# Kernel optimization log

Measured on AMD Instinct MI355X. Metric: run time of the kernel, lower is better.

## Reference

```python
import jax, jax.numpy as jnp
import numpy as np

M = 1536   # rows (users)
N = 1536   # cols (items)
P_ROW = 4  # Chebyshev order over rows
P_COL = 4  # Chebyshev order over cols
OUT = 32   # out_channels_GCCN


def cheb_basis(L, order):
    """Stack of Chebyshev polynomials T_k(L), shape (order+1, n, n)."""
    n = L.shape[0]
    Ts = [jnp.eye(n, dtype=L.dtype)]
    if order > 0:
        Ts.append(L)
    for _ in range(2, order + 1):
        Ts.append(2.0 * (L @ Ts[-1]) - Ts[-2])
    return jnp.stack(Ts)


def setup_inputs() -> dict:
    key = jax.random.key(0)
    kx, kr, kc, kt = jax.random.split(key, 4)
    x = jax.random.normal(kx, (1, M, N), dtype=jnp.float32)
    # Scaled symmetric 'Laplacians' with spectral radius < 1 so the
    # Chebyshev recursion stays numerically stable.
    Ar = jax.random.normal(kr, (M, M), dtype=jnp.float32)
    Lr = (Ar + Ar.T) / (4.0 * jnp.sqrt(jnp.float32(M)))
    Ac = jax.random.normal(kc, (N, N), dtype=jnp.float32)
    Lc = (Ac + Ac.T) / (4.0 * jnp.sqrt(jnp.float32(N)))
    theta = jax.random.normal(kt, (P_ROW + 1, P_COL + 1, 1, OUT), dtype=jnp.float32) * 0.05
    bias = jnp.zeros((OUT,), dtype=jnp.float32)
    return {"x": x, "Lr": Lr, "Lc": Lc, "theta": theta, "bias": bias}


def reference(x, Lr, Lc, theta, bias):
    # Chebyshev bases: Tr (p_row+1, M, M), Tc (p_col+1, N, N)
    Tr = cheb_basis(Lr, theta.shape[0] - 1)
    Tc = cheb_basis(Lc, theta.shape[1] - 1)
    # Stage 1: row transform -> (i, c, M, N)
    x_row = jnp.einsum('imp,cpn->icmn', Tr, x)
    # Stage 2: col transform -> (i, j, c, M, N)
    basis_feats = jnp.einsum('icmn,jnk->ijcmk', x_row, Tc)
    # Stage 3: bilinear weights -> (OUT, M, N)
    out = jnp.einsum('ijcmn,ijco->omn', basis_feats, theta)
    return out + bias[:, None, None]
```

## Files before the change

### kernel.cpp

```cpp
#include <hip/hip_runtime.h>
#include <hip/hip_bf16.h>


#define NDIM 1536
#define PM (NDIM * NDIM)
#define NK 24

typedef __attribute__((ext_vector_type(8))) short bf16x8;
typedef __attribute__((ext_vector_type(4))) float f32x4;

__device__ inline void gload_lds16(const void* g, void* l) {
  __builtin_amdgcn_global_load_lds(
      (const __attribute__((address_space(1))) void*)g,
      (__attribute__((address_space(3))) void*)l, 16, 0, 0);
}

__device__ inline unsigned short f2bf(float f) {
  __hip_bfloat16 h = __float2bfloat16(f);
  return *reinterpret_cast<unsigned short*>(&h);
}
__device__ inline float bf2f(unsigned short u) {
  return __uint_as_float((unsigned)u << 16);
}

struct ZSet {
  const unsigned short* A;
  const unsigned short* Bt;
  unsigned short* out;
  const unsigned short* Cp;
  int mode;
};
struct ZSet4 { ZSet z[4]; };

#define PH_MID()                                       \
  do {                                                 \
    asm volatile("" ::: "memory");                     \
    __builtin_amdgcn_s_barrier();                      \
    asm volatile("s_waitcnt lgkmcnt(0)" ::: "memory"); \
    __builtin_amdgcn_sched_barrier(0);                 \
    __builtin_amdgcn_s_setprio(1);                     \
  } while (0)

#define PH_END()                                       \
  do {                                                 \
    __builtin_amdgcn_s_setprio(0);                     \
    asm volatile("" ::: "memory");                     \
    __builtin_amdgcn_s_barrier();                      \
  } while (0)

__global__ __launch_bounds__(512, 2) void gemm256_k(ZSet4 zs) {
  const ZSet zp = zs.z[blockIdx.z];
  __shared__ __align__(16) unsigned short As[2][2][8192];
  __shared__ __align__(16) unsigned short Bs[2][2][8192];
  const int tid = threadIdx.x;
  const int lane = tid & 63;
  const int wave = tid >> 6;
  const int wm = wave >> 2, wn = wave & 3;
  const int gm0 = blockIdx.y * 256;
  const int jn = blockIdx.x / 6;
  const int nloc0 = (blockIdx.x % 6) * 256;
  const int q = lane >> 4;
  const int rowl = lane & 15;
  const unsigned short* Ab = zp.A;
  const unsigned short* Btb = zp.Bt + (size_t)jn * PM;
  unsigned short* outb = zp.out + (size_t)jn * 5 * PM;

  bf16x8 a[4][2];
  bf16x8 b0[2][2], b1[2][2];
  f32x4 acc00[4][2] = {}, acc01[4][2] = {}, acc10[4][2] = {}, acc11[4][2] = {};

  auto stageA = [&](int buf, int h, int kt) {
#pragma unroll
    for (int l = 0; l < 2; ++l) {
      const int o = (wave * 2 + l) * 1024 + lane * 16;
      const int wms = o >> 13;
      const int r = (o >> 7) & 63;
      const int s = (o >> 4) & 7;
      const unsigned short* src =
          Ab + (size_t)(gm0 + wms * 128 + h * 64 + r) * NDIM + kt * 64 +
          ((s ^ (r & 7)) << 3);
      gload_lds16(src, &As[buf][h][(wave * 2 + l) * 512]);
    }
  };
  auto stageB = [&](int buf, int h, int kt) {
#pragma unroll
    for (int l = 0; l < 2; ++l) {
      const int o = (wave * 2 + l) * 1024 + lane * 16;
      const int wns = o >> 12;
      const int r = (o >> 7) & 31;
      const int s = (o >> 4) & 7;
      const unsigned short* src =
          Btb + (size_t)(nloc0 + wns * 64 + h * 32 + r) * NDIM + kt * 64 +
          ((s ^ (r & 7)) << 3);
      gload_lds16(src, &Bs[buf][h][(wave * 2 + l) * 512]);
    }
  };
  auto loadA = [&](int buf, int h) {
#pragma unroll
    for (int mt = 0; mt < 4; ++mt) {
      const int lr = mt * 16 + rowl;
#pragma unroll
      for (int ks = 0; ks < 2; ++ks) {
        const int s0 = ks * 4 + q;
        a[mt][ks] = *(const bf16x8*)&As[buf][h][wm * 4096 + lr * 64 +
                                                ((s0 ^ (lr & 7)) << 3)];
      }
    }
  };
  auto loadB = [&](bf16x8 (&bb)[2][2], int buf, int h) {
#pragma unroll
    for (int nt = 0; nt < 2; ++nt) {
      const int lr = nt * 16 + rowl;
#pragma unroll
      for (int ks = 0; ks < 2; ++ks) {
        const int s0 = ks * 4 + q;
        bb[nt][ks] = *(const bf16x8*)&Bs[buf][h][wn * 2048 + lr * 64 +
                                                 ((s0 ^ (lr & 7)) << 3)];
      }
    }
  };
  auto mfma16 = [&](f32x4 (&ac)[4][2], bf16x8 (&bb)[2][2]) {
#pragma unroll
    for (int mt = 0; mt < 4; ++mt)
#pragma unroll
      for (int nt = 0; nt < 2; ++nt)
#pragma unroll
        for (int ks = 0; ks < 2; ++ks)
          ac[mt][nt] = __builtin_amdgcn_mfma_f32_16x16x32_bf16(
              a[mt][ks], bb[nt][ks], ac[mt][nt], 0, 0, 0);
  };

  stageA(0, 0, 0); stageB(0, 0, 0); stageB(0, 1, 0); stageA(0, 1, 0);
  stageA(1, 0, 1); stageB(1, 0, 1); stageB(1, 1, 1);
  asm volatile("s_waitcnt vmcnt(6)" ::: "memory");
  __builtin_amdgcn_s_barrier();

  auto ktile = [&](int kt, int b) {
    loadA(b, 0);
    loadB(b0, b, 0);
    if (kt + 1 < NK) stageA(b ^ 1, 1, kt + 1);
    PH_MID();
    mfma16(acc00, b0);
    PH_END();
    loadB(b1, b, 1);
    if (kt + 2 < NK) stageA(b, 0, kt + 2);
    PH_MID();
    mfma16(acc01, b1);
    PH_END();
    loadA(b, 1);
    if (kt + 2 < NK) stageB(b, 0, kt + 2);
    PH_MID();
    mfma16(acc11, b1);
    PH_END();
    if (kt + 2 < NK) {
      stageB(b, 1, kt + 2);
      asm volatile("s_waitcnt vmcnt(6)" ::: "memory");
    } else {
      asm volatile("s_waitcnt vmcnt(0)" ::: "memory");
    }
    PH_MID();
    mfma16(acc10, b0);
    PH_END();
  };
  for (int kt = 0; kt < NK; kt += 2) {
    ktile(kt, 0);
    ktile(kt + 1, 1);
  }

  auto writeQ = [&](f32x4 (&ac)[4][2], int mh, int nh) {
#pragma unroll
    for (int mt = 0; mt < 4; ++mt)
#pragma unroll
      for (int nt = 0; nt < 2; ++nt)
#pragma unroll
        for (int v = 0; v < 4; ++v) {
          const int row = gm0 + wm * 128 + mh * 64 + mt * 16 + q * 4 + v;
          const int col = nloc0 + wn * 64 + nh * 32 + nt * 16 + rowl;
          const size_t idx = (size_t)row * NDIM + col;
          float val = ac[mt][nt][v];
          if (zp.mode == 1) val = 2.0f * val - bf2f(zp.Cp[idx]);
          if (zp.mode == 2) val = 2.0f * val - (row == col ? 1.0f : 0.0f);
          outb[idx] = f2bf(val);
        }
  };
  writeQ(acc00, 0, 0);
  writeQ(acc01, 0, 1);
  writeQ(acc11, 1, 1);
  writeQ(acc10, 1, 0);
}

__global__ __launch_bounds__(256) void gemm_k(ZSet4 zs) {
  const ZSet zp = zs.z[blockIdx.z];
  __shared__ __align__(16) unsigned short As[128 * 32];
  __shared__ __align__(16) unsigned short Bs[128 * 32];
  const int tid = threadIdx.x;
  const int lane = tid & 63;
  const int wave = tid >> 6;
  const int wm = wave >> 1, wn = wave & 1;
  const int gm0 = blockIdx.y * 128;
  const int jn = blockIdx.x / 12;
  const int nloc0 = (blockIdx.x % 12) * 128;
  const int q = lane >> 4;
  const int rowl = lane & 15;

  const unsigned short* Btb = zp.Bt + (size_t)jn * PM;
  unsigned short* outb = zp.out + (size_t)jn * 5 * PM;

  f32x4 acc[4][4] = {};

  for (int k0 = 0; k0 < NDIM; k0 += 32) {
#pragma unroll
    for (int l = 0; l < 2; ++l) {
      int f = l * 256 + wave * 64 + lane;
      int r = f >> 2, kc = f & 3;
      const unsigned short* ga = zp.A + (size_t)(gm0 + r) * NDIM + k0 + kc * 8;
      const unsigned short* gb = Btb + (size_t)(nloc0 + r) * NDIM + k0 + kc * 8;
      unsigned short* la = &As[(size_t)(l * 256 + wave * 64) * 8];
      unsigned short* lb = &Bs[(size_t)(l * 256 + wave * 64) * 8];
      gload_lds16(ga, la);
      gload_lds16(gb, lb);
    }
    __syncthreads();
    bf16x8 af[4], bfv[4];
#pragma unroll
    for (int t = 0; t < 4; ++t) {
      af[t] = *(const bf16x8*)&As[(wm * 64 + t * 16 + rowl) * 32 + q * 8];
      bfv[t] = *(const bf16x8*)&Bs[(wn * 64 + t * 16 + rowl) * 32 + q * 8];
    }
#pragma unroll
    for (int mt = 0; mt < 4; ++mt)
#pragma unroll
      for (int nt = 0; nt < 4; ++nt)
        acc[mt][nt] = __builtin_amdgcn_mfma_f32_16x16x32_bf16(
            af[mt], bfv[nt], acc[mt][nt], 0, 0, 0);
    __syncthreads();
  }

#pragma unroll
  for (int mt = 0; mt < 4; ++mt) {
#pragma unroll
    for (int nt = 0; nt < 4; ++nt) {
#pragma unroll
      for (int v = 0; v < 4; ++v) {
        int row = gm0 + wm * 64 + mt * 16 + q * 4 + v;
        int col = nloc0 + wn * 64 + nt * 16 + rowl;
        size_t idx = (size_t)row * NDIM + col;
        float val = acc[mt][nt][v];
        if (zp.mode == 1) val = 2.0f * val - bf2f(zp.Cp[idx]);
        if (zp.mode == 2) val = 2.0f * val - (row == col ? 1.0f : 0.0f);
        outb[idx] = f2bf(val);
      }
    }
  }
}

__global__ void transpose_f2b(const float* __restrict__ in,
                              unsigned short* __restrict__ out16,
                              unsigned short* __restrict__ outS) {
  __shared__ float tile[32][33];
  int bx = blockIdx.x, by = blockIdx.y;
  int tx = threadIdx.x;
#pragma unroll
  for (int r = threadIdx.y; r < 32; r += 8) {
    float v = in[(size_t)(by * 32 + r) * NDIM + bx * 32 + tx];
    tile[r][tx] = v;
    outS[(size_t)(by * 32 + r) * NDIM + bx * 32 + tx] = f2bf(v);
  }
  __syncthreads();
  int ox = by * 32 + tx;
#pragma unroll
  for (int r = threadIdx.y; r < 32; r += 8)
    out16[(size_t)(bx * 32 + r) * NDIM + ox] = f2bf(tile[tx][r]);
}

__global__ void cast_bf16_k(const float* __restrict__ in,
                            unsigned short* __restrict__ out) {
  int i = (blockIdx.x * 256 + threadIdx.x) * 4;
  float4 v = *(const float4*)(in + i);
  ushort4 r;
  r.x = f2bf(v.x); r.y = f2bf(v.y); r.z = f2bf(v.z); r.w = f2bf(v.w);
  *(ushort4*)(out + i) = r;
}

__global__ __launch_bounds__(256, 2) void combine_k(
    const unsigned short* __restrict__ Z,
    const float* __restrict__ theta,
    const float* __restrict__ bias,
    float* __restrict__ out) {
  __shared__ float th[800];
  __shared__ float bs[32];
  const int tid = threadIdx.x;
  for (int t = tid; t < 800; t += 256) th[t] = theta[t];
  if (tid < 32) bs[tid] = bias[tid];
  __syncthreads();

  const size_t p0 = (size_t)(blockIdx.x * 256 + tid) * 4;
  float z[25][4];
#pragma unroll
  for (int c = 0; c < 25; ++c) {
    uint2 u = *(const uint2*)(Z + (size_t)c * PM + p0);
    z[c][0] = __uint_as_float(u.x << 16);
    z[c][1] = __uint_as_float(u.x & 0xffff0000u);
    z[c][2] = __uint_as_float(u.y << 16);
    z[c][3] = __uint_as_float(u.y & 0xffff0000u);
  }
#pragma unroll 2
  for (int o = 0; o < 32; ++o) {
    float b = bs[o];
    float a0 = b, a1 = b, a2 = b, a3 = b;
#pragma unroll
    for (int c = 0; c < 25; ++c) {
      const int i = c % 5, j = c / 5;
      float t = th[i * 160 + j * 32 + o];
      a0 += t * z[c][0];
      a1 += t * z[c][1];
      a2 += t * z[c][2];
      a3 += t * z[c][3];
    }
    float4 w; w.x = a0; w.y = a1; w.z = a2; w.w = a3;
    *(float4*)(out + (size_t)o * PM + p0) = w;
  }
}

extern "C" void kernel_launch(void* const* d_in, const int* in_sizes, int n_in,
                              void* d_out, int out_size, void* d_ws, size_t ws_size,
                              hipStream_t stream) {
  (void)in_sizes; (void)n_in; (void)out_size; (void)ws_size;
  const float* X = (const float*)d_in[0];
  const float* Lr = (const float*)d_in[1];
  const float* Lc = (const float*)d_in[2];
  const float* theta = (const float*)d_in[3];
  const float* bias = (const float*)d_in[4];
  float* out = (float*)d_out;

  unsigned short* Zall = (unsigned short*)d_ws;
  unsigned short* Tr = Zall + (size_t)25 * PM;
  unsigned short* Tc = Tr + (size_t)4 * PM;
  unsigned short* Xt = Tc + (size_t)4 * PM;

  unsigned short* Tr0 = Tr;                 unsigned short* Tc0 = Tc;
  unsigned short* Tr1 = Tr + (size_t)PM;    unsigned short* Tc1 = Tc + (size_t)PM;
  unsigned short* Tr2 = Tr + (size_t)2*PM;  unsigned short* Tc2 = Tc + (size_t)2*PM;
  unsigned short* Tr3 = Tr + (size_t)3*PM;  unsigned short* Tc3 = Tc + (size_t)3*PM;

  cast_bf16_k<<<PM / 1024, 256, 0, stream>>>(Lr, Tr0);
  cast_bf16_k<<<PM / 1024, 256, 0, stream>>>(Lc, Tc0);
  transpose_f2b<<<dim3(48, 48), dim3(32, 8), 0, stream>>>(X, Xt, Zall);

  {
    ZSet4 a{};
    a.z[0] = {Tr0, Tr0, Tr1, nullptr, 2};
    a.z[1] = {Tc0, Tc0, Tc1, nullptr, 2};
    gemm_k<<<dim3(12, 12, 2), 256, 0, stream>>>(a);
  }
  {
    ZSet4 a{};
    a.z[0] = {Tr0, Tr1, Tr2, Tr0, 1};
    a.z[1] = {Tr1, Tr1, Tr3, nullptr, 2};
    a.z[2] = {Tc0, Tc1, Tc2, Tc0, 1};
    a.z[3] = {Tc1, Tc1, Tc3, nullptr, 2};
    gemm_k<<<dim3(12, 12, 4), 256, 0, stream>>>(a);
  }
  {
    ZSet4 a{};
    a.z[0] = {Tr, Xt, Zall + (size_t)PM, nullptr, 0};
    gemm256_k<<<dim3(6, 24, 1), 512, 0, stream>>>(a);
  }
  {
    ZSet4 a{};
    a.z[0] = {Zall, Tc0, Zall + (size_t)5 * PM, nullptr, 0};
    gemm256_k<<<dim3(24, 30, 1), 512, 0, stream>>>(a);
  }

  combine_k<<<PM / 1024, 256, 0, stream>>>(Zall, theta, bias, out);
}
```

Baseline: 716.5 us.

## Swizzle GEMM blocks across XCDs, merge cast launches, slim combine registers

Result: slower. 993.9 us (+38.7%).

```diff
diff --git a/kernel.cpp b/kernel.cpp
--- a/kernel.cpp
+++ b/kernel.cpp
@@ -32,6 +32,16 @@
 };
 struct ZSet4 { ZSet z[4]; };
 
+__device__ inline void xcd_swizzle(int& bx, int& by) {
+  const int gx = gridDim.x;
+  const int nwg = gx * gridDim.y;
+  int lin = by * gx + bx;
+  const int nper = nwg >> 3;
+  lin = (lin & 7) * nper + (lin >> 3);
+  bx = lin % gx;
+  by = lin / gx;
+}
+
 #define PH_MID()                                       \
   do {                                                 \
     asm volatile("" ::: "memory");                     \
@@ -52,13 +62,15 @@
   const ZSet zp = zs.z[blockIdx.z];
   __shared__ __align__(16) unsigned short As[2][2][8192];
   __shared__ __align__(16) unsigned short Bs[2][2][8192];
+  int bswx = blockIdx.x, bswy = blockIdx.y;
+  xcd_swizzle(bswx, bswy);
   const int tid = threadIdx.x;
   const int lane = tid & 63;
   const int wave = tid >> 6;
   const int wm = wave >> 2, wn = wave & 3;
-  const int gm0 = blockIdx.y * 256;
-  const int jn = blockIdx.x / 6;
-  const int nloc0 = (blockIdx.x % 6) * 256;
+  const int gm0 = bswy * 256;
+  const int jn = bswx / 6;
+  const int nloc0 = (bswx % 6) * 256;
   const int q = lane >> 4;
   const int rowl = lane & 15;
   const unsigned short* Ab = zp.A;
@@ -193,13 +205,15 @@
   const ZSet zp = zs.z[blockIdx.z];
   __shared__ __align__(16) unsigned short As[128 * 32];
   __shared__ __align__(16) unsigned short Bs[128 * 32];
+  int bswx = blockIdx.x, bswy = blockIdx.y;
+  xcd_swizzle(bswx, bswy);
   const int tid = threadIdx.x;
   const int lane = tid & 63;
   const int wave = tid >> 6;
   const int wm = wave >> 1, wn = wave & 1;
-  const int gm0 = blockIdx.y * 128;
-  const int jn = blockIdx.x / 12;
-  const int nloc0 = (blockIdx.x % 12) * 128;
+  const int gm0 = bswy * 128;
+  const int jn = bswx / 12;
+  const int nloc0 = (bswx % 12) * 128;
   const int q = lane >> 4;
   const int rowl = lane & 15;
 
@@ -273,8 +287,12 @@
     out16[(size_t)(bx * 32 + r) * NDIM + ox] = f2bf(tile[tx][r]);
 }
 
-__global__ void cast_bf16_k(const float* __restrict__ in,
-                            unsigned short* __restrict__ out) {
+__global__ void cast2_bf16_k(const float* __restrict__ inA,
+                             unsigned short* __restrict__ outA,
+                             const float* __restrict__ inB,
+                             unsigned short* __restrict__ outB) {
+  const float* in = blockIdx.y ? inB : inA;
+  unsigned short* out = blockIdx.y ? outB : outA;
   int i = (blockIdx.x * 256 + threadIdx.x) * 4;
   float4 v = *(const float4*)(in + i);
   ushort4 r;
@@ -282,7 +300,7 @@
   *(ushort4*)(out + i) = r;
 }
 
-__global__ __launch_bounds__(256, 2) void combine_k(
+__global__ __launch_bounds__(256, 4) void combine_k(
     const unsigned short* __restrict__ Z,
     const float* __restrict__ theta,
     const float* __restrict__ bias,
@@ -295,16 +313,12 @@
   __syncthreads();
 
   const size_t p0 = (size_t)(blockIdx.x * 256 + tid) * 4;
-  float z[25][4];
-#pragma unroll
-  for (int c = 0; c < 25; ++c) {
-    uint2 u = *(const uint2*)(Z + (size_t)c * PM + p0);
-    z[c][0] = __uint_as_float(u.x << 16);
-    z[c][1] = __uint_as_float(u.x & 0xffff0000u);
-    z[c][2] = __uint_as_float(u.y << 16);
-    z[c][3] = __uint_as_float(u.y & 0xffff0000u);
-  }
-#pragma unroll 2
+  uint2 zr[25];
+#pragma unroll
+  for (int c = 0; c < 25; ++c)
+    zr[c] = *(const uint2*)(Z + (size_t)c * PM + p0);
+
+#pragma unroll 4
   for (int o = 0; o < 32; ++o) {
     float b = bs[o];
     float a0 = b, a1 = b, a2 = b, a3 = b;
@@ -312,10 +326,10 @@
     for (int c = 0; c < 25; ++c) {
       const int i = c % 5, j = c / 5;
       float t = th[i * 160 + j * 32 + o];
-      a0 += t * z[c][0];
-      a1 += t * z[c][1];
-      a2 += t * z[c][2];
-      a3 += t * z[c][3];
+      a0 += t * __uint_as_float(zr[c].x << 16);
+      a1 += t * __uint_as_float(zr[c].x & 0xffff0000u);
+      a2 += t * __uint_as_float(zr[c].y << 16);
+      a3 += t * __uint_as_float(zr[c].y & 0xffff0000u);
     }
     float4 w; w.x = a0; w.y = a1; w.z = a2; w.w = a3;
     *(float4*)(out + (size_t)o * PM + p0) = w;
@@ -343,8 +357,7 @@
   unsigned short* Tr2 = Tr + (size_t)2*PM;  unsigned short* Tc2 = Tc + (size_t)2*PM;
   unsigned short* Tr3 = Tr + (size_t)3*PM;  unsigned short* Tc3 = Tc + (size_t)3*PM;
 
-  cast_bf16_k<<<PM / 1024, 256, 0, stream>>>(Lr, Tr0);
-  cast_bf16_k<<<PM / 1024, 256, 0, stream>>>(Lc, Tc0);
+  cast2_bf16_k<<<dim3(PM / 1024, 2), 256, 0, stream>>>(Lr, Tr0, Lc, Tc0);
   transpose_f2b<<<dim3(48, 48), dim3(32, 8), 0, stream>>>(X, Xt, Zall);
 
   {
```
